# Optimization experiments

Measured on AMD Instinct MI355X. Metric: run time of the kernel, lower is better.

The kernel has to match this reference:

```python
import jax, jax.numpy as jnp
import numpy as np

B, Li, Lh, Lq, K, H, W = 256, 2, 150, 10, 40, 64, 64

def _conv(x, w, pad):
    # NCHW conv, stride 1, symmetric padding
    return jax.lax.conv_general_dilated(
        x, w, window_strides=(1, 1), padding=[(pad, pad), (pad, pad)],
        dimension_numbers=('NCHW', 'OIHW', 'NCHW'))

def setup_inputs() -> dict:
    key = jax.random.key(0)
    ks = jax.random.split(key, 8)
    g = lambda k, shape, s: jax.random.normal(k, shape, jnp.float32) * s
    return {
        'X':  g(ks[0], (B, Li, H, W), 1.0),
        'Wh': g(ks[1], (Lh, Li, 3, 3), 0.1),   # h conv weight
        'bh': jnp.zeros((Lh,), jnp.float32),     # h conv bias
        'Wr': g(ks[2], (1, Lh, 1, 1), 0.1),      # r conv (1x1, no bias)
        'Wq': g(ks[3], (Lq, 1, 3, 3), 0.1),      # q conv (no bias)
        'w':  g(ks[4], (Lq, 1, 3, 3), 0.1),      # transition weight (torch inits zeros; randomized for nontrivial grads)
        'Wc': g(ks[5], (1, H * W), 0.02),        # critic linear weight
        'bc': jnp.zeros((1,), jnp.float32),      # critic linear bias
    }

def reference(X, Wh, bh, Wr, Wq, w, Wc, bc):
    h = _conv(X, Wh, 1) + bh[None, :, None, None]   # [B,Lh,H,W]
    r = _conv(h, Wr, 0)                              # [B,1,H,W]
    q = _conv(r, Wq, 1)                              # [B,Lq,H,W]
    Wcat = jnp.concatenate([Wq, w], axis=1)          # [Lq,2,3,3]
    def step(q, _):
        v = q.max(axis=1, keepdims=True)             # [B,1,H,W]
        qn = _conv(jnp.concatenate([r, v], axis=1), Wcat, 1)
        return qn, None
    # torch: K-1 loop iterations + 1 final => K concat-convs after initial q
    q, _ = jax.lax.scan(step, q, None, length=K)
    v = q.max(axis=1, keepdims=True)
    critic = v.reshape(-1, H * W) @ Wc.T + bc        # [B,1]
    return critic, q.reshape(-1, Lq * H * W)
```

## Files before the change

### kernel.cpp

```cpp
#include <hip/hip_runtime.h>
#include <hip/hip_bf16.h>

#define HH 64
#define WW 64
#define S  68
#define PH 66
#define NLQ 10
#define NK 40

__global__ __launch_bounds__(512, 2) void vin_fused(
    const float* __restrict__ X,
    const float* __restrict__ Wh,
    const float* __restrict__ bh,
    const float* __restrict__ Wr,
    const float* __restrict__ Wq,
    const float* __restrict__ wtr,
    const float* __restrict__ Wc,
    const float* __restrict__ bc,
    float* __restrict__ out)
{
  __shared__ float vb[2][PH * S];
  __shared__ float rb[PH * S];
  __shared__ float Wef[19];
  __shared__ float Wqs[90];
  __shared__ float Wts[90];
  __shared__ float red[8];

  const int b  = blockIdx.x;
  const int t  = threadIdx.x;
  const int x  = t & 63;
  const int yg = t >> 6;
  const int y0 = yg << 3;

  {
    float* vbf = &vb[0][0];
    for (int i = t; i < 2 * PH * S; i += 512) vbf[i] = 0.f;
    for (int i = t; i < PH * S; i += 512) rb[i] = 0.f;
  }
  __syncthreads();

  const float* Xb = X + (size_t)b * (2 * HH * WW);
  for (int i = t; i < HH * WW; i += 512) {
    const int yy = i >> 6, xx = i & 63;
    vb[0][(yy + 1) * S + xx + 1] = Xb[i];
    vb[1][(yy + 1) * S + xx + 1] = Xb[HH * WW + i];
  }
  if (t < 19) {
    float s = 0.f;
    if (t < 18) {
      const int ci = t / 9, k = t - ci * 9;
      for (int c = 0; c < 150; ++c)
        s += Wr[c] * Wh[c * 18 + ci * 9 + k];
    } else {
      for (int c = 0; c < 150; ++c) s += Wr[c] * bh[c];
    }
    Wef[t] = s;
  } else if (t < 109) {
    Wqs[t - 19] = Wq[t - 19];
  } else if (t < 199) {
    Wts[t - 109] = wtr[t - 109];
  }
  __syncthreads();

  {
    float We[19];
#pragma unroll
    for (int i = 0; i < 19; ++i) We[i] = Wef[i];
#pragma unroll
    for (int j = 0; j < 8; ++j) {
      const int tb = (y0 + j) * S + x;
      float s = We[18];
#pragma unroll
      for (int dy = 0; dy < 3; ++dy)
#pragma unroll
        for (int dx = 0; dx < 3; ++dx) {
          const int idx = tb + dy * S + dx;
          s = fmaf(vb[0][idx], We[dy * 3 + dx], s);
          s = fmaf(vb[1][idx], We[9 + dy * 3 + dx], s);
        }
      rb[tb + S + 1] = s;
    }
  }
  __syncthreads();

  float q0r[8][NLQ];
  {
    float Wqf[90];
#pragma unroll
    for (int i = 0; i < 90; ++i) Wqf[i] = Wqs[i];
#pragma unroll
    for (int j = 0; j < 8; ++j) {
      const int tb = (y0 + j) * S + x;
      float p[9];
#pragma unroll
      for (int dy = 0; dy < 3; ++dy)
#pragma unroll
        for (int dx = 0; dx < 3; ++dx) p[dy * 3 + dx] = rb[tb + dy * S + dx];
      float m = -3.0e38f;
#pragma unroll
      for (int l = 0; l < NLQ; ++l) {
        float s = 0.f;
#pragma unroll
        for (int k = 0; k < 9; ++k) s = fmaf(Wqf[l * 9 + k], p[k], s);
        q0r[j][l] = s;
        m = fmaxf(m, s);
      }
      vb[0][tb + S + 1] = m;
    }
  }
  __syncthreads();

  float Wt[90];
#pragma unroll
  for (int i = 0; i < 90; ++i) Wt[i] = Wts[i];

  const int base0 = y0 * S + x;

  auto step = [&](const float* __restrict__ vin, float* __restrict__ vout) {
    float a0 = vin[base0],     a1 = vin[base0 + 1],     a2 = vin[base0 + 2];
    float b0 = vin[base0 + S], b1 = vin[base0 + S + 1], b2 = vin[base0 + S + 2];
#pragma unroll
    for (int j = 0; j < 8; ++j) {
      const int rbx = base0 + (j + 2) * S;
      float c0 = vin[rbx], c1 = vin[rbx + 1], c2 = vin[rbx + 2];
      float m = -3.0e38f;
#pragma unroll
      for (int l = 0; l < NLQ; ++l) {
        float s = q0r[j][l];
        s = fmaf(Wt[l * 9 + 0], a0, s);
        s = fmaf(Wt[l * 9 + 1], a1, s);
        s = fmaf(Wt[l * 9 + 2], a2, s);
        s = fmaf(Wt[l * 9 + 3], b0, s);
        s = fmaf(Wt[l * 9 + 4], b1, s);
        s = fmaf(Wt[l * 9 + 5], b2, s);
        s = fmaf(Wt[l * 9 + 6], c0, s);
        s = fmaf(Wt[l * 9 + 7], c1, s);
        s = fmaf(Wt[l * 9 + 8], c2, s);
        m = fmaxf(m, s);
      }
      vout[base0 + (j + 1) * S + 1] = m;
      a0 = b0; a1 = b1; a2 = b2;
      b0 = c0; b1 = c1; b2 = c2;
    }
    __syncthreads();
  };

  for (int s2 = 0; s2 < 19; ++s2) { step(vb[0], vb[1]); step(vb[1], vb[0]); }
  step(vb[0], vb[1]);

  float wcv[8];
#pragma unroll
  for (int j = 0; j < 8; ++j) wcv[j] = Wc[(y0 + j) * WW + x];

  float* qo = out + 256 + (size_t)b * (NLQ * HH * WW) + y0 * WW + x;
  float acc = 0.f;
  {
    const float* vin = vb[1];
    float a0 = vin[base0],     a1 = vin[base0 + 1],     a2 = vin[base0 + 2];
    float b0 = vin[base0 + S], b1 = vin[base0 + S + 1], b2 = vin[base0 + S + 2];
#pragma unroll
    for (int j = 0; j < 8; ++j) {
      const int rbx = base0 + (j + 2) * S;
      float c0 = vin[rbx], c1 = vin[rbx + 1], c2 = vin[rbx + 2];
      float m = -3.0e38f;
#pragma unroll
      for (int l = 0; l < NLQ; ++l) {
        float s = q0r[j][l];
        s = fmaf(Wt[l * 9 + 0], a0, s);
        s = fmaf(Wt[l * 9 + 1], a1, s);
        s = fmaf(Wt[l * 9 + 2], a2, s);
        s = fmaf(Wt[l * 9 + 3], b0, s);
        s = fmaf(Wt[l * 9 + 4], b1, s);
        s = fmaf(Wt[l * 9 + 5], b2, s);
        s = fmaf(Wt[l * 9 + 6], c0, s);
        s = fmaf(Wt[l * 9 + 7], c1, s);
        s = fmaf(Wt[l * 9 + 8], c2, s);
        qo[l * (HH * WW) + j * WW] = s;
        m = fmaxf(m, s);
      }
      acc = fmaf(m, wcv[j], acc);
      a0 = b0; a1 = b1; a2 = b2;
      b0 = c0; b1 = c1; b2 = c2;
    }
  }

#pragma unroll
  for (int off = 32; off > 0; off >>= 1) acc += __shfl_down(acc, off);
  if ((t & 63) == 0) red[yg] = acc;
  __syncthreads();
  if (t == 0) {
    float s = bc[0];
#pragma unroll
    for (int i = 0; i < 8; ++i) s += red[i];
    out[b] = s;
  }
}

extern "C" void kernel_launch(void* const* d_in, const int* in_sizes, int n_in,
                              void* d_out, int out_size, void* d_ws, size_t ws_size,
                              hipStream_t stream) {
  (void)n_in; (void)out_size; (void)d_ws; (void)ws_size;
  const float* X   = (const float*)d_in[0];
  const float* Wh  = (const float*)d_in[1];
  const float* bh  = (const float*)d_in[2];
  const float* Wr  = (const float*)d_in[3];
  const float* Wq  = (const float*)d_in[4];
  const float* wtr = (const float*)d_in[5];
  const float* Wc  = (const float*)d_in[6];
  const float* bc  = (const float*)d_in[7];
  float* out = (float*)d_out;

  const int B = in_sizes[0] / (2 * HH * WW);
  vin_fused<<<B, 512, 0, stream>>>(X, Wh, bh, Wr, Wq, wtr, Wc, bc, out);
}
```

Measured before the change: 170.2 us.

## Use 1024-thread blocks with 4 rows per thread and scalar-loaded weights

Doubles the block to 1024 threads so each thread computes 4 output rows instead of 8, which roughly halves the per-thread q0r register state. Transition and Wq weights are now read straight from global memory through a uniform pointer (an asm constraint pins it to SGPRs) rather than staged in shared memory and copied into 90 VGPRs. Loop order is changed to iterate over channels in the outer loop with a sliding window held in registers. The aim is to cut VGPR pressure and raise wave occupancy on the serial 40-step recurrence. In exchange the launch bound assumes 4 blocks of 1024 threads, and more waves now contend at each of the 40 barriers.

```diff
diff --git a/kernel.cpp b/kernel.cpp
--- a/kernel.cpp
+++ b/kernel.cpp
@@ -1,14 +1,13 @@
 #include <hip/hip_runtime.h>
-#include <hip/hip_bf16.h>
 
 #define HH 64
 #define WW 64
 #define S  68
 #define PH 66
 #define NLQ 10
-#define NK 40
-
-__global__ __launch_bounds__(512, 2) void vin_fused(
+#define NR 4
+
+__global__ __launch_bounds__(1024, 4) void vin_fused(
     const float* __restrict__ X,
     const float* __restrict__ Wh,
     const float* __restrict__ bh,
@@ -22,25 +21,24 @@
   __shared__ float vb[2][PH * S];
   __shared__ float rb[PH * S];
   __shared__ float Wef[19];
-  __shared__ float Wqs[90];
-  __shared__ float Wts[90];
-  __shared__ float red[8];
+  __shared__ float red[16];
 
   const int b  = blockIdx.x;
   const int t  = threadIdx.x;
   const int x  = t & 63;
   const int yg = t >> 6;
-  const int y0 = yg << 3;
+  const int y0 = yg * NR;
+  const int base0 = y0 * S + x;
 
   {
     float* vbf = &vb[0][0];
-    for (int i = t; i < 2 * PH * S; i += 512) vbf[i] = 0.f;
-    for (int i = t; i < PH * S; i += 512) rb[i] = 0.f;
+    for (int i = t; i < 2 * PH * S; i += 1024) vbf[i] = 0.f;
+    for (int i = t; i < PH * S; i += 1024) rb[i] = 0.f;
   }
   __syncthreads();
 
   const float* Xb = X + (size_t)b * (2 * HH * WW);
-  for (int i = t; i < HH * WW; i += 512) {
+  for (int i = t; i < HH * WW; i += 1024) {
     const int yy = i >> 6, xx = i & 63;
     vb[0][(yy + 1) * S + xx + 1] = Xb[i];
     vb[1][(yy + 1) * S + xx + 1] = Xb[HH * WW + i];
@@ -48,17 +46,11 @@
   if (t < 19) {
     float s = 0.f;
     if (t < 18) {
-      const int ci = t / 9, k = t - ci * 9;
-      for (int c = 0; c < 150; ++c)
-        s += Wr[c] * Wh[c * 18 + ci * 9 + k];
+      for (int c = 0; c < 150; ++c) s += Wr[c] * Wh[c * 18 + t];
     } else {
       for (int c = 0; c < 150; ++c) s += Wr[c] * bh[c];
     }
     Wef[t] = s;
-  } else if (t < 109) {
-    Wqs[t - 19] = Wq[t - 19];
-  } else if (t < 199) {
-    Wts[t - 109] = wtr[t - 109];
   }
   __syncthreads();
 
@@ -67,8 +59,8 @@
 #pragma unroll
     for (int i = 0; i < 19; ++i) We[i] = Wef[i];
 #pragma unroll
-    for (int j = 0; j < 8; ++j) {
-      const int tb = (y0 + j) * S + x;
+    for (int j = 0; j < NR; ++j) {
+      const int tb = base0 + j * S;
       float s = We[18];
 #pragma unroll
       for (int dy = 0; dy < 3; ++dy)
@@ -83,115 +75,136 @@
   }
   __syncthreads();
 
-  float q0r[8][NLQ];
-  {
-    float Wqf[90];
-#pragma unroll
-    for (int i = 0; i < 90; ++i) Wqf[i] = Wqs[i];
-#pragma unroll
-    for (int j = 0; j < 8; ++j) {
-      const int tb = (y0 + j) * S + x;
-      float p[9];
-#pragma unroll
-      for (int dy = 0; dy < 3; ++dy)
-#pragma unroll
-        for (int dx = 0; dx < 3; ++dx) p[dy * 3 + dx] = rb[tb + dy * S + dx];
-      float m = -3.0e38f;
-#pragma unroll
-      for (int l = 0; l < NLQ; ++l) {
+  float q0r[NR][NLQ];
+  {
+    float win[NR + 2][3];
+#pragma unroll
+    for (int rr = 0; rr < NR + 2; ++rr) {
+      const int a = base0 + rr * S;
+      win[rr][0] = rb[a]; win[rr][1] = rb[a + 1]; win[rr][2] = rb[a + 2];
+    }
+    float m[NR];
+#pragma unroll
+    for (int j = 0; j < NR; ++j) m[j] = -3.0e38f;
+    const float* wq = Wq;
+#pragma unroll
+    for (int l = 0; l < NLQ; ++l) {
+      const float w0 = wq[l * 9 + 0], w1 = wq[l * 9 + 1], w2 = wq[l * 9 + 2];
+      const float w3 = wq[l * 9 + 3], w4 = wq[l * 9 + 4], w5 = wq[l * 9 + 5];
+      const float w6 = wq[l * 9 + 6], w7 = wq[l * 9 + 7], w8 = wq[l * 9 + 8];
+#pragma unroll
+      for (int j = 0; j < NR; ++j) {
         float s = 0.f;
-#pragma unroll
-        for (int k = 0; k < 9; ++k) s = fmaf(Wqf[l * 9 + k], p[k], s);
+        s = fmaf(w0, win[j][0], s);
+        s = fmaf(w1, win[j][1], s);
+        s = fmaf(w2, win[j][2], s);
+        s = fmaf(w3, win[j + 1][0], s);
+        s = fmaf(w4, win[j + 1][1], s);
+        s = fmaf(w5, win[j + 1][2], s);
+        s = fmaf(w6, win[j + 2][0], s);
+        s = fmaf(w7, win[j + 2][1], s);
+        s = fmaf(w8, win[j + 2][2], s);
         q0r[j][l] = s;
-        m = fmaxf(m, s);
+        m[j] = fmaxf(m[j], s);
       }
-      vb[0][tb + S + 1] = m;
-    }
-  }
-  __syncthreads();
-
-  float Wt[90];
-#pragma unroll
-  for (int i = 0; i < 90; ++i) Wt[i] = Wts[i];
-
-  const int base0 = y0 * S + x;
+    }
+#pragma unroll
+    for (int j = 0; j < NR; ++j) vb[0][base0 + (j + 1) * S + 1] = m[j];
+  }
+  __syncthreads();
 
   auto step = [&](const float* __restrict__ vin, float* __restrict__ vout) {
-    float a0 = vin[base0],     a1 = vin[base0 + 1],     a2 = vin[base0 + 2];
-    float b0 = vin[base0 + S], b1 = vin[base0 + S + 1], b2 = vin[base0 + S + 2];
-#pragma unroll
-    for (int j = 0; j < 8; ++j) {
-      const int rbx = base0 + (j + 2) * S;
-      float c0 = vin[rbx], c1 = vin[rbx + 1], c2 = vin[rbx + 2];
-      float m = -3.0e38f;
-#pragma unroll
-      for (int l = 0; l < NLQ; ++l) {
+    float win[NR + 2][3];
+#pragma unroll
+    for (int rr = 0; rr < NR + 2; ++rr) {
+      const int a = base0 + rr * S;
+      win[rr][0] = vin[a]; win[rr][1] = vin[a + 1]; win[rr][2] = vin[a + 2];
+    }
+    float m[NR];
+#pragma unroll
+    for (int j = 0; j < NR; ++j) m[j] = -3.0e38f;
+    const float* wp = wtr;
+    asm volatile("" : "+s"(wp));
+#pragma unroll
+    for (int l = 0; l < NLQ; ++l) {
+      const float w0 = wp[l * 9 + 0], w1 = wp[l * 9 + 1], w2 = wp[l * 9 + 2];
+      const float w3 = wp[l * 9 + 3], w4 = wp[l * 9 + 4], w5 = wp[l * 9 + 5];
+      const float w6 = wp[l * 9 + 6], w7 = wp[l * 9 + 7], w8 = wp[l * 9 + 8];
+#pragma unroll
+      for (int j = 0; j < NR; ++j) {
         float s = q0r[j][l];
-        s = fmaf(Wt[l * 9 + 0], a0, s);
-        s = fmaf(Wt[l * 9 + 1], a1, s);
-        s = fmaf(Wt[l * 9 + 2], a2, s);
-        s = fmaf(Wt[l * 9 + 3], b0, s);
-        s = fmaf(Wt[l * 9 + 4], b1, s);
-        s = fmaf(Wt[l * 9 + 5], b2, s);
-        s = fmaf(Wt[l * 9 + 6], c0, s);
-        s = fmaf(Wt[l * 9 + 7], c1, s);
-        s = fmaf(Wt[l * 9 + 8], c2, s);
-        m = fmaxf(m, s);
+        s = fmaf(w0, win[j][0], s);
+        s = fmaf(w1, win[j][1], s);
+        s = fmaf(w2, win[j][2], s);
+        s = fmaf(w3, win[j + 1][0], s);
+        s = fmaf(w4, win[j + 1][1], s);
+        s = fmaf(w5, win[j + 1][2], s);
+        s = fmaf(w6, win[j + 2][0], s);
+        s = fmaf(w7, win[j + 2][1], s);
+        s = fmaf(w8, win[j + 2][2], s);
+        m[j] = fmaxf(m[j], s);
       }
-      vout[base0 + (j + 1) * S + 1] = m;
-      a0 = b0; a1 = b1; a2 = b2;
-      b0 = c0; b1 = c1; b2 = c2;
-    }
+    }
+#pragma unroll
+    for (int j = 0; j < NR; ++j) vout[base0 + (j + 1) * S + 1] = m[j];
     __syncthreads();
   };
 
   for (int s2 = 0; s2 < 19; ++s2) { step(vb[0], vb[1]); step(vb[1], vb[0]); }
   step(vb[0], vb[1]);
 
-  float wcv[8];
-#pragma unroll
-  for (int j = 0; j < 8; ++j) wcv[j] = Wc[(y0 + j) * WW + x];
+  float wcv[NR];
+#pragma unroll
+  for (int j = 0; j < NR; ++j) wcv[j] = Wc[(y0 + j) * WW + x];
 
   float* qo = out + 256 + (size_t)b * (NLQ * HH * WW) + y0 * WW + x;
   float acc = 0.f;
   {
     const float* vin = vb[1];
-    float a0 = vin[base0],     a1 = vin[base0 + 1],     a2 = vin[base0 + 2];
-    float b0 = vin[base0 + S], b1 = vin[base0 + S + 1], b2 = vin[base0 + S + 2];
-#pragma unroll
-    for (int j = 0; j < 8; ++j) {
-      const int rbx = base0 + (j + 2) * S;
-      float c0 = vin[rbx], c1 = vin[rbx + 1], c2 = vin[rbx + 2];
-      float m = -3.0e38f;
-#pragma unroll
-      for (int l = 0; l < NLQ; ++l) {
+    float win[NR + 2][3];
+#pragma unroll
+    for (int rr = 0; rr < NR + 2; ++rr) {
+      const int a = base0 + rr * S;
+      win[rr][0] = vin[a]; win[rr][1] = vin[a + 1]; win[rr][2] = vin[a + 2];
+    }
+    float m[NR];
+#pragma unroll
+    for (int j = 0; j < NR; ++j) m[j] = -3.0e38f;
+    const float* wp = wtr;
+    asm volatile("" : "+s"(wp));
+#pragma unroll
+    for (int l = 0; l < NLQ; ++l) {
+      const float w0 = wp[l * 9 + 0], w1 = wp[l * 9 + 1], w2 = wp[l * 9 + 2];
+      const float w3 = wp[l * 9 + 3], w4 = wp[l * 9 + 4], w5 = wp[l * 9 + 5];
+      const float w6 = wp[l * 9 + 6], w7 = wp[l * 9 + 7], w8 = wp[l * 9 + 8];
+#pragma unroll
+      for (int j = 0; j < NR; ++j) {
         float s = q0r[j][l];
-        s = fmaf(Wt[l * 9 + 0], a0, s);
-        s = fmaf(Wt[l * 9 + 1], a1, s);
-        s = fmaf(Wt[l * 9 + 2], a2, s);
-        s = fmaf(Wt[l * 9 + 3], b0, s);
-        s = fmaf(Wt[l * 9 + 4], b1, s);
-        s = fmaf(Wt[l * 9 + 5], b2, s);
-        s = fmaf(Wt[l * 9 + 6], c0, s);
-        s = fmaf(Wt[l * 9 + 7], c1, s);
-        s = fmaf(Wt[l * 9 + 8], c2, s);
+        s = fmaf(w0, win[j][0], s);
+        s = fmaf(w1, win[j][1], s);
+        s = fmaf(w2, win[j][2], s);
+        s = fmaf(w3, win[j + 1][0], s);
+        s = fmaf(w4, win[j + 1][1], s);
+        s = fmaf(w5, win[j + 1][2], s);
+        s = fmaf(w6, win[j + 2][0], s);
+        s = fmaf(w7, win[j + 2][1], s);
+        s = fmaf(w8, win[j + 2][2], s);
         qo[l * (HH * WW) + j * WW] = s;
-        m = fmaxf(m, s);
+        m[j] = fmaxf(m[j], s);
       }
-      acc = fmaf(m, wcv[j], acc);
-      a0 = b0; a1 = b1; a2 = b2;
-      b0 = c0; b1 = c1; b2 = c2;
-    }
+    }
+#pragma unroll
+    for (int j = 0; j < NR; ++j) acc = fmaf(m[j], wcv[j], acc);
   }
 
 #pragma unroll
   for (int off = 32; off > 0; off >>= 1) acc += __shfl_down(acc, off);
-  if ((t & 63) == 0) red[yg] = acc;
+  if (x == 0) red[yg] = acc;
   __syncthreads();
   if (t == 0) {
     float s = bc[0];
 #pragma unroll
-    for (int i = 0; i < 8; ++i) s += red[i];
+    for (int i = 0; i < 16; ++i) s += red[i];
     out[b] = s;
   }
 }
@@ -211,5 +224,5 @@
   float* out = (float*)d_out;
 
   const int B = in_sizes[0] / (2 * HH * WW);
-  vin_fused<<<B, 512, 0, stream>>>(X, Wh, bh, Wr, Wq, wtr, Wc, bc, out);
+  vin_fused<<<B, 1024, 0, stream>>>(X, Wh, bh, Wr, Wq, wtr, Wc, bc, out);
 }
```

New measurement: 213.0 us. +25.1%, slower.
